# Performance work log

Hardware: AMD Instinct MI355X
Metric: run time of the kernel (lower is better)

Reference implementation:

```python
import jax, jax.numpy as jnp
import numpy as np

G = 250          # grid_size hardcoded in forward
CENTER = G // 2  # 125
K = 1000         # max steps of torch.linspace(r, 2, int((2-r)*500)+1) for r in (0,1)
PAD = 1          # kernel_size // 2 for kernel_size=3
PRED = 10


def rasterize(lidar):
    """Vectorized polar_to_cartesian: lidar [B,360] -> binary grid [B,1,G,G]."""
    B = lidar.shape[0]
    dtype = lidar.dtype
    angles = jnp.linspace(0.0, 2.0 * jnp.pi, 360)            # [360]
    r = lidar                                                 # [B,360]
    valid_r = (r > 0.0) & (r < 1.0)
    # steps = int((2-r)*500) + 1  (positive -> floor == trunc)
    n = jnp.floor((2.0 - r) * 500.0).astype(jnp.int32) + 1   # [B,360], in [501,1000]
    k = jnp.arange(K, dtype=jnp.int32)                        # [K]
    denom = jnp.maximum(n - 1, 1).astype(dtype)
    # torch.linspace(r, 2, n): mag_k = r + k*(2-r)/(n-1)
    mag = r[..., None] + k.astype(dtype) * (2.0 - r)[..., None] / denom[..., None]  # [B,360,K]
    step_ok = k[None, None, :] < n[..., None]
    x = mag * jnp.cos(angles)[None, :, None]
    y = mag * jnp.sin(angles)[None, :, None]
    # int(.) truncates toward zero
    xg = jnp.trunc(CENTER + x * 100.0).astype(jnp.int32)
    yg = jnp.trunc(CENTER + y * 100.0).astype(jnp.int32)
    inb = (xg >= 0) & (xg < G) & (yg >= 0) & (yg < G)
    valid = valid_r[..., None] & step_ok & inb               # [B,360,K]
    idx = jnp.where(valid, yg * G + xg, G * G)               # invalid -> sentinel slot
    flat = jnp.zeros((B, G * G + 1), dtype=dtype)
    flat = flat.at[jnp.arange(B)[:, None, None], idx].max(valid.astype(dtype))
    return flat[:, : G * G].reshape(B, 1, G, G)


def conv2d(x, w, b):
    y = jax.lax.conv_general_dilated(
        x, w, window_strides=(1, 1), padding=[(PAD, PAD), (PAD, PAD)],
        dimension_numbers=("NCHW", "OIHW", "NCHW"))
    return y + b[None, :, None, None]


def linear(x, w, b):  # torch convention: w [out,in]
    return x @ w.T + b


def setup_inputs() -> dict:
    key = jax.random.key(0)
    ks = jax.random.split(key, 18)
    B = 8
    HW, HL = 64, 64  # hidden_size_wind, hidden_size_lidar
    conv_out = 32 * G * G  # 2,000,000

    def w(k, shape, fan_in):
        return jax.random.normal(k, shape, dtype=jnp.float32) / np.float32(np.sqrt(fan_in))

    return {
        "lidar": jax.random.uniform(ks[0], (B, 360), dtype=jnp.float32),
        "wind": jax.random.normal(ks[1], (B, 2), dtype=jnp.float32),
        "w_wind1": w(ks[2], (HW, 2), 2), "b_wind1": jnp.zeros((HW,), jnp.float32),
        "w_wind2": w(ks[3], (HW, HW), HW), "b_wind2": jnp.zeros((HW,), jnp.float32),
        "w_wind3": w(ks[4], (HW, HW), HW), "b_wind3": jnp.zeros((HW,), jnp.float32),
        "conv1_w": w(ks[5], (16, 1, 3, 3), 9), "conv1_b": jnp.zeros((16,), jnp.float32),
        "conv2_w": w(ks[6], (32, 16, 3, 3), 16 * 9), "conv2_b": jnp.zeros((32,), jnp.float32),
        "fc1_w": w(ks[7], (HL, conv_out + HW), conv_out + HW), "fc1_b": jnp.zeros((HL,), jnp.float32),
        "fc2_w": w(ks[8], (HL // 2, HL), HL), "fc2_b": jnp.zeros((HL // 2,), jnp.float32),
        "fc3_w": w(ks[9], (2 * PRED * PRED, HL // 2), HL // 2), "fc3_b": jnp.zeros((2 * PRED * PRED,), jnp.float32),
    }


def reference(lidar, wind, w_wind1, b_wind1, w_wind2, b_wind2, w_wind3, b_wind3,
              conv1_w, conv1_b, conv2_w, conv2_b, fc1_w, fc1_b, fc2_w, fc2_b, fc3_w, fc3_b):
    B = lidar.shape[0]
    img = rasterize(lidar)                                    # [B,1,250,250]
    wnd = jax.nn.relu(linear(wind, w_wind1, b_wind1))
    wnd = jax.nn.relu(linear(wnd, w_wind2, b_wind2))
    wnd = jax.nn.relu(linear(wnd, w_wind3, b_wind3))          # [B,64]
    h = jax.nn.relu(conv2d(img, conv1_w, conv1_b))            # [B,16,250,250]
    h = jax.nn.relu(conv2d(h, conv2_w, conv2_b))              # [B,32,250,250]
    h = h.reshape(B, -1)                                      # [B,2000000]
    x = jnp.concatenate([h, wnd], axis=1)
    x = jax.nn.relu(linear(x, fc1_w, fc1_b))
    x = jax.nn.relu(linear(x, fc2_w, fc2_b))
    x = linear(x, fc3_w, fc3_b)
    return x.reshape(B, PRED, PRED, 2)
```

## Files before the change

### kernel.cpp

```cpp
#include <hip/hip_runtime.h>

#define G 250
#define GG 62500
#define NB 8
#define HFEAT 2000000
#define W1STRIDE 2000064
#define NCH 7813
#define SPAN 16

__global__ void k_raster(const float* __restrict__ lidar, float* __restrict__ img) {
    int idx = blockIdx.x * blockDim.x + threadIdx.x;
    if (idx >= NB * 360 * 1000) return;
    int k = idx % 1000;
    int ba = idx / 1000;
    int a = ba % 360;
    int b = ba / 360;
    float r = lidar[ba];
    if (!(r > 0.0f && r < 1.0f)) return;
    float tmr = __fsub_rn(2.0f, r);
    int n = (int)floorf(__fmul_rn(tmr, 500.0f)) + 1;
    if (k >= n) return;
    float denom = (float)(n - 1);
    const float delta = 6.2831855f / 359.0f;
    float angle = __fmul_rn((float)a, delta);
    float mag = __fadd_rn(r, __fdiv_rn(__fmul_rn((float)k, tmr), denom));
    float c = cosf(angle);
    float s = sinf(angle);
    float px = __fadd_rn(125.0f, __fmul_rn(__fmul_rn(mag, c), 100.0f));
    float py = __fadd_rn(125.0f, __fmul_rn(__fmul_rn(mag, s), 100.0f));
    int xg = (int)px;
    int yg = (int)py;
    if (xg >= 0 && xg < G && yg >= 0 && yg < G)
        img[b * GG + yg * G + xg] = 1.0f;
}

__global__ __launch_bounds__(256) void k_conv12(const float* __restrict__ img,
                                                const float* __restrict__ w1,
                                                const float* __restrict__ b1,
                                                const float* __restrict__ w2,
                                                const float* __restrict__ b2,
                                                float* __restrict__ h) {
    __shared__ float s_img[20][37];
    __shared__ float s_c1[16][18][35];
    __shared__ float s_w2[4608];
    __shared__ float s_w1[144];
    __shared__ float s_b1[16];
    int t = threadIdx.x;
    int bx = blockIdx.x, by = blockIdx.y, b = blockIdx.z;
    for (int i = t; i < 4608; i += 256) s_w2[i] = w2[i];
    if (t < 144) s_w1[t] = w1[t];
    if (t < 16) s_b1[t] = b1[t];
    int x0 = bx * 32 - 1, y0 = by * 16 - 1;
    for (int i = t; i < 20 * 36; i += 256) {
        int r = i / 36, c = i - r * 36;
        int gy = y0 - 1 + r, gx = x0 - 1 + c;
        float v = 0.0f;
        if (gy >= 0 && gy < G && gx >= 0 && gx < G) v = img[b * GG + gy * G + gx];
        s_img[r][c] = v;
    }
    __syncthreads();
    for (int i = t; i < 612; i += 256) {
        int yy = i / 34, xx = i - yy * 34;
        int gy = y0 + yy, gx = x0 + xx;
        bool inb = (gy >= 0 && gy < G && gx >= 0 && gx < G);
        float iv[9];
#pragma unroll
        for (int dy = 0; dy < 3; ++dy)
#pragma unroll
            for (int dx = 0; dx < 3; ++dx)
                iv[dy * 3 + dx] = s_img[yy + dy][xx + dx];
#pragma unroll
        for (int co = 0; co < 16; ++co) {
            float a = s_b1[co];
#pragma unroll
            for (int k = 0; k < 9; ++k) a = fmaf(iv[k], s_w1[co * 9 + k], a);
            s_c1[co][yy][xx] = inb ? fmaxf(a, 0.0f) : 0.0f;
        }
    }
    __syncthreads();
    int pg = t & 63;
    int cog = t >> 6;
    int ry = pg >> 2;
    int rx = (pg & 3) * 8;
    float acc[8][8];
#pragma unroll
    for (int i = 0; i < 8; ++i)
#pragma unroll
        for (int j = 0; j < 8; ++j) acc[i][j] = 0.0f;
    for (int ci = 0; ci < 16; ++ci) {
        float in[3][10];
#pragma unroll
        for (int dy = 0; dy < 3; ++dy)
#pragma unroll
            for (int xx = 0; xx < 10; ++xx)
                in[dy][xx] = s_c1[ci][ry + dy][rx + xx];
#pragma unroll
        for (int coi = 0; coi < 8; ++coi) {
            const float* wp = &s_w2[(cog * 8 + coi) * 144 + ci * 9];
            float w0 = wp[0], w1v = wp[1], w2v = wp[2], w3 = wp[3], w4 = wp[4],
                  w5 = wp[5], w6 = wp[6], w7 = wp[7], w8 = wp[8];
#pragma unroll
            for (int px = 0; px < 8; ++px) {
                float a = acc[coi][px];
                a = fmaf(in[0][px],     w0,  a);
                a = fmaf(in[0][px + 1], w1v, a);
                a = fmaf(in[0][px + 2], w2v, a);
                a = fmaf(in[1][px],     w3,  a);
                a = fmaf(in[1][px + 1], w4,  a);
                a = fmaf(in[1][px + 2], w5,  a);
                a = fmaf(in[2][px],     w6,  a);
                a = fmaf(in[2][px + 1], w7,  a);
                a = fmaf(in[2][px + 2], w8,  a);
                acc[coi][px] = a;
            }
        }
    }
    int y = by * 16 + ry;
    if (y < G) {
#pragma unroll
        for (int coi = 0; coi < 8; ++coi) {
            int co = cog * 8 + coi;
            float bv = b2[co];
#pragma unroll
            for (int px = 0; px < 8; ++px) {
                int x = bx * 32 + rx + px;
                if (x < G)
                    h[((size_t)(b * 32 + co)) * GG + y * G + x] =
                        fmaxf(acc[coi][px] + bv, 0.0f);
            }
        }
    }
}

__global__ __launch_bounds__(256) void k_fc1(const float* __restrict__ h,
                                             const float* __restrict__ W1,
                                             float* __restrict__ accout) {
    int t = threadIdx.x;
    int w = t >> 6;
    int l = t & 63;
    int s = blockIdx.x >> 1;
    int g = ((blockIdx.x & 1) << 2) | w;
    int cbeg = s * SPAN;
    if (cbeg >= NCH) return;
    int cend = min(cbeg + SPAN, NCH);

    const float* wrow[8];
#pragma unroll
    for (int oi = 0; oi < 8; ++oi)
        wrow[oi] = W1 + (size_t)(g * 8 + oi) * W1STRIDE;

    float acc[64];
#pragma unroll
    for (int i = 0; i < 64; ++i) acc[i] = 0.0f;

    for (int c = cbeg; c < cend; ++c) {
        int j = c * 256 + l * 4;
        if (j < HFEAT) {
            float4 hv[8], wv[8];
#pragma unroll
            for (int oi = 0; oi < 8; ++oi)
                wv[oi] = *(const float4*)(wrow[oi] + j);
#pragma unroll
            for (int b = 0; b < 8; ++b)
                hv[b] = *(const float4*)(h + (size_t)b * HFEAT + j);
#pragma unroll
            for (int oi = 0; oi < 8; ++oi) {
#pragma unroll
                for (int b = 0; b < 8; ++b) {
                    float a = acc[oi * 8 + b];
                    a = fmaf(wv[oi].x, hv[b].x, a);
                    a = fmaf(wv[oi].y, hv[b].y, a);
                    a = fmaf(wv[oi].z, hv[b].z, a);
                    a = fmaf(wv[oi].w, hv[b].w, a);
                    acc[oi * 8 + b] = a;
                }
            }
        }
    }

    int cnt = 64;
#pragma unroll
    for (int st = 0; st < 6; ++st) {
        int half = cnt >> 1;
        bool up = (l >> st) & 1;
#pragma unroll
        for (int i = 0; i < half; ++i) {
            float send = up ? acc[i] : acc[i + half];
            float keep = up ? acc[i + half] : acc[i];
            float recv = __shfl_xor(send, 1 << st, 64);
            acc[i] = keep + recv;
        }
        cnt = half;
    }
    unsigned vi = __brev((unsigned)l) >> 26;
    atomicAdd(&accout[g * 64 + vi], acc[0]);
}

__global__ void k_final(const float* __restrict__ wind,
                        const float* __restrict__ ww1, const float* __restrict__ wb1,
                        const float* __restrict__ ww2, const float* __restrict__ wb2,
                        const float* __restrict__ ww3, const float* __restrict__ wb3,
                        const float* __restrict__ W1, const float* __restrict__ fb1,
                        const float* __restrict__ acc,
                        const float* __restrict__ w2, const float* __restrict__ b2,
                        const float* __restrict__ w3, const float* __restrict__ b3,
                        float* __restrict__ out) {
    __shared__ float s1[8][64], s2[8][64], f1[8][64], f2[8][32];
    int t = threadIdx.x;
    if (t < 64) {
        for (int b = 0; b < 8; ++b) {
            float v = wb1[t] + ww1[t * 2] * wind[b * 2] + ww1[t * 2 + 1] * wind[b * 2 + 1];
            s1[b][t] = fmaxf(v, 0.0f);
        }
    }
    __syncthreads();
    if (t < 64) {
        for (int b = 0; b < 8; ++b) {
            float v = wb2[t];
            for (int k = 0; k < 64; ++k) v = fmaf(s1[b][k], ww2[t * 64 + k], v);
            s2[b][t] = fmaxf(v, 0.0f);
        }
    }
    __syncthreads();
    if (t < 64) {
        for (int b = 0; b < 8; ++b) {
            float v = wb3[t];
            for (int k = 0; k < 64; ++k) v = fmaf(s2[b][k], ww3[t * 64 + k], v);
            s1[b][t] = fmaxf(v, 0.0f);
        }
    }
    __syncthreads();
    if (t < 64) {
        for (int b = 0; b < 8; ++b) {
            float v = fb1[t] + acc[t * 8 + b];
            const float* wrow = W1 + (size_t)t * W1STRIDE + HFEAT;
            for (int k = 0; k < 64; ++k) v = fmaf(s1[b][k], wrow[k], v);
            f1[b][t] = fmaxf(v, 0.0f);
        }
    }
    __syncthreads();
    if (t < 32) {
        for (int b = 0; b < 8; ++b) {
            float v = b2[t];
            for (int k = 0; k < 64; ++k) v = fmaf(f1[b][k], w2[t * 64 + k], v);
            f2[b][t] = fmaxf(v, 0.0f);
        }
    }
    __syncthreads();
    if (t < 200) {
        for (int b = 0; b < 8; ++b) {
            float v = b3[t];
            for (int k = 0; k < 32; ++k) v = fmaf(f2[b][k], w3[t * 32 + k], v);
            out[b * 200 + t] = v;
        }
    }
}

extern "C" void kernel_launch(void* const* d_in, const int* in_sizes, int n_in,
                              void* d_out, int out_size, void* d_ws, size_t ws_size,
                              hipStream_t stream) {
    const float* lidar = (const float*)d_in[0];
    const float* wind  = (const float*)d_in[1];
    const float* ww1 = (const float*)d_in[2];
    const float* wb1 = (const float*)d_in[3];
    const float* ww2 = (const float*)d_in[4];
    const float* wb2 = (const float*)d_in[5];
    const float* ww3 = (const float*)d_in[6];
    const float* wb3 = (const float*)d_in[7];
    const float* c1w = (const float*)d_in[8];
    const float* c1b = (const float*)d_in[9];
    const float* c2w = (const float*)d_in[10];
    const float* c2b = (const float*)d_in[11];
    const float* fw1 = (const float*)d_in[12];
    const float* fb1 = (const float*)d_in[13];
    const float* fw2 = (const float*)d_in[14];
    const float* fb2 = (const float*)d_in[15];
    const float* fw3 = (const float*)d_in[16];
    const float* fb3 = (const float*)d_in[17];
    float* out = (float*)d_out;

    float* ws  = (float*)d_ws;
    float* img = ws;
    float* h   = ws + 500000;
    float* acc = ws + 16500000;

    hipMemsetAsync(img, 0, 500000 * sizeof(float), stream);
    hipMemsetAsync(acc, 0, 512 * sizeof(float), stream);

    k_raster<<<(NB * 360 * 1000 + 255) / 256, 256, 0, stream>>>(lidar, img);
    dim3 g2(8, 16, NB);
    k_conv12<<<g2, 256, 0, stream>>>(img, c1w, c1b, c2w, c2b, h);
    int nblk = 2 * ((NCH + SPAN - 1) / SPAN);
    k_fc1<<<nblk, 256, 0, stream>>>(h, fw1, acc);
    k_final<<<1, 256, 0, stream>>>(wind, ww1, wb1, ww2, wb2, ww3, wb3,
                                   fw1, fb1, acc, fw2, fb2, fw3, fb3, out);
}
```

Before: 241.5 us.

## Remap fc1 blocks so warps share one output group and stream weights nontemporally

```diff
diff --git a/kernel.cpp b/kernel.cpp
--- a/kernel.cpp
+++ b/kernel.cpp
@@ -6,7 +6,9 @@
 #define HFEAT 2000000
 #define W1STRIDE 2000064
 #define NCH 7813
-#define SPAN 16
+#define SPANC 64
+
+typedef float f4v __attribute__((ext_vector_type(4)));
 
 __global__ void k_raster(const float* __restrict__ lidar, float* __restrict__ img) {
     int idx = blockIdx.x * blockDim.x + threadIdx.x;
@@ -138,11 +140,10 @@
     int t = threadIdx.x;
     int w = t >> 6;
     int l = t & 63;
-    int s = blockIdx.x >> 1;
-    int g = ((blockIdx.x & 1) << 2) | w;
-    int cbeg = s * SPAN;
-    if (cbeg >= NCH) return;
-    int cend = min(cbeg + SPAN, NCH);
+    int g = blockIdx.x & 7;
+    int s = blockIdx.x >> 3;
+    int cbase = s * SPANC;
+    if (cbase >= NCH) return;
 
     const float* wrow[8];
 #pragma unroll
@@ -153,13 +154,16 @@
 #pragma unroll
     for (int i = 0; i < 64; ++i) acc[i] = 0.0f;
 
-    for (int c = cbeg; c < cend; ++c) {
+    for (int q = 0; q < 16; ++q) {
+        int c = cbase + q * 4 + w;
+        if (c >= NCH) break;
         int j = c * 256 + l * 4;
         if (j < HFEAT) {
-            float4 hv[8], wv[8];
+            f4v wv[8];
+            float4 hv[8];
 #pragma unroll
             for (int oi = 0; oi < 8; ++oi)
-                wv[oi] = *(const float4*)(wrow[oi] + j);
+                wv[oi] = __builtin_nontemporal_load((const f4v*)(wrow[oi] + j));
 #pragma unroll
             for (int b = 0; b < 8; ++b)
                 hv[b] = *(const float4*)(h + (size_t)b * HFEAT + j);
@@ -168,10 +172,10 @@
 #pragma unroll
                 for (int b = 0; b < 8; ++b) {
                     float a = acc[oi * 8 + b];
-                    a = fmaf(wv[oi].x, hv[b].x, a);
-                    a = fmaf(wv[oi].y, hv[b].y, a);
-                    a = fmaf(wv[oi].z, hv[b].z, a);
-                    a = fmaf(wv[oi].w, hv[b].w, a);
+                    a = fmaf(wv[oi][0], hv[b].x, a);
+                    a = fmaf(wv[oi][1], hv[b].y, a);
+                    a = fmaf(wv[oi][2], hv[b].z, a);
+                    a = fmaf(wv[oi][3], hv[b].w, a);
                     acc[oi * 8 + b] = a;
                 }
             }
@@ -290,8 +294,8 @@
     k_raster<<<(NB * 360 * 1000 + 255) / 256, 256, 0, stream>>>(lidar, img);
     dim3 g2(8, 16, NB);
     k_conv12<<<g2, 256, 0, stream>>>(img, c1w, c1b, c2w, c2b, h);
-    int nblk = 2 * ((NCH + SPAN - 1) / SPAN);
-    k_fc1<<<nblk, 256, 0, stream>>>(h, fw1, acc);
+    int nspan = (NCH + SPANC - 1) / SPANC;
+    k_fc1<<<8 * nspan, 256, 0, stream>>>(h, fw1, acc);
     k_final<<<1, 256, 0, stream>>>(wind, ww1, wb1, ww2, wb2, ww3, wb3,
                                    fw1, fb1, acc, fw2, fb2, fw3, fb3, out);
 }
```

New measurement: 264.3 us. 9.5% more time.

## Double-buffer fc1 chunk loads and merge output groups into one 512-thread block

Applied to the files above, without the earlier changes.

```diff
diff --git a/kernel.cpp b/kernel.cpp
--- a/kernel.cpp
+++ b/kernel.cpp
@@ -132,15 +132,41 @@
     }
 }
 
-__global__ __launch_bounds__(256) void k_fc1(const float* __restrict__ h,
-                                             const float* __restrict__ W1,
-                                             float* __restrict__ accout) {
+#define LOADCH(WV, HV, c)                                                       \
+    {                                                                           \
+        int j = (c) * 256 + l * 4;                                              \
+        _Pragma("unroll")                                                       \
+        for (int oi = 0; oi < 8; ++oi)                                          \
+            WV[oi] = *(const float4*)(wrow[oi] + j);                            \
+        bool ok = j < HFEAT;                                                    \
+        _Pragma("unroll")                                                       \
+        for (int b = 0; b < 8; ++b)                                             \
+            HV[b] = ok ? *(const float4*)(h + (size_t)b * HFEAT + j) : f4z;     \
+    }
+
+#define FMACH(WV, HV)                                                           \
+    {                                                                           \
+        _Pragma("unroll")                                                       \
+        for (int oi = 0; oi < 8; ++oi) {                                        \
+            _Pragma("unroll")                                                   \
+            for (int b = 0; b < 8; ++b) {                                       \
+                float a = acc[oi * 8 + b];                                      \
+                a = fmaf(WV[oi].x, HV[b].x, a);                                 \
+                a = fmaf(WV[oi].y, HV[b].y, a);                                 \
+                a = fmaf(WV[oi].z, HV[b].z, a);                                 \
+                a = fmaf(WV[oi].w, HV[b].w, a);                                 \
+                acc[oi * 8 + b] = a;                                            \
+            }                                                                   \
+        }                                                                       \
+    }
+
+__global__ __launch_bounds__(512, 2) void k_fc1(const float* __restrict__ h,
+                                                const float* __restrict__ W1,
+                                                float* __restrict__ accout) {
     int t = threadIdx.x;
-    int w = t >> 6;
+    int g = t >> 6;
     int l = t & 63;
-    int s = blockIdx.x >> 1;
-    int g = ((blockIdx.x & 1) << 2) | w;
-    int cbeg = s * SPAN;
+    int cbeg = blockIdx.x * SPAN;
     if (cbeg >= NCH) return;
     int cend = min(cbeg + SPAN, NCH);
 
@@ -153,30 +179,18 @@
 #pragma unroll
     for (int i = 0; i < 64; ++i) acc[i] = 0.0f;
 
-    for (int c = cbeg; c < cend; ++c) {
-        int j = c * 256 + l * 4;
-        if (j < HFEAT) {
-            float4 hv[8], wv[8];
-#pragma unroll
-            for (int oi = 0; oi < 8; ++oi)
-                wv[oi] = *(const float4*)(wrow[oi] + j);
-#pragma unroll
-            for (int b = 0; b < 8; ++b)
-                hv[b] = *(const float4*)(h + (size_t)b * HFEAT + j);
-#pragma unroll
-            for (int oi = 0; oi < 8; ++oi) {
-#pragma unroll
-                for (int b = 0; b < 8; ++b) {
-                    float a = acc[oi * 8 + b];
-                    a = fmaf(wv[oi].x, hv[b].x, a);
-                    a = fmaf(wv[oi].y, hv[b].y, a);
-                    a = fmaf(wv[oi].z, hv[b].z, a);
-                    a = fmaf(wv[oi].w, hv[b].w, a);
-                    acc[oi * 8 + b] = a;
-                }
-            }
-        }
-    }
+    const float4 f4z = make_float4(0.f, 0.f, 0.f, 0.f);
+    float4 wa[8], ha[8], wb[8], hb[8];
+
+    LOADCH(wa, ha, cbeg)
+    int c = cbeg;
+    for (; c + 2 <= cend; c += 2) {
+        LOADCH(wb, hb, c + 1)
+        FMACH(wa, ha)
+        if (c + 2 < cend) LOADCH(wa, ha, c + 2)
+        FMACH(wb, hb)
+    }
+    if (c < cend) FMACH(wa, ha)
 
     int cnt = 64;
 #pragma unroll
@@ -290,8 +304,8 @@
     k_raster<<<(NB * 360 * 1000 + 255) / 256, 256, 0, stream>>>(lidar, img);
     dim3 g2(8, 16, NB);
     k_conv12<<<g2, 256, 0, stream>>>(img, c1w, c1b, c2w, c2b, h);
-    int nblk = 2 * ((NCH + SPAN - 1) / SPAN);
-    k_fc1<<<nblk, 256, 0, stream>>>(h, fw1, acc);
+    int nblk = (NCH + SPAN - 1) / SPAN;
+    k_fc1<<<nblk, 512, 0, stream>>>(h, fw1, acc);
     k_final<<<1, 256, 0, stream>>>(wind, ww1, wb1, ww2, wb2, ww3, wb3,
                                    fw1, fb1, acc, fw2, fb2, fw3, fb3, out);
 }
```

Result: slower. 394.8 us (+63.5%).
